# Kernel optimization log

Hardware: AMD Instinct MI355X
Metric: run time of the kernel (lower is better)

Reference implementation:

```python
import jax, jax.numpy as jnp
import numpy as np

N_NODES = 100000
N_EDGES = 1600000
N_GRAPHS = 512
F_IN = 128
HID = 128
N_CLS = 10


def setup_inputs() -> dict:
    key = jax.random.key(0)
    ks = jax.random.split(key, 12)
    x = jax.random.normal(ks[0], (N_NODES, F_IN), dtype=jnp.float32)
    edge_index = jax.random.randint(ks[1], (2, N_EDGES), 0, N_NODES, dtype=jnp.int64)
    batch = jnp.sort(jax.random.randint(ks[2], (N_NODES,), 0, N_GRAPHS, dtype=jnp.int64))
    def glorot(k, shape):
        lim = float(np.sqrt(6.0 / (shape[0] + shape[1])))
        return jax.random.uniform(k, shape, jnp.float32, -lim, lim)
    return {
        "x": x, "edge_index": edge_index, "batch": batch,
        "W1": glorot(ks[3], (F_IN, HID)), "b1": jnp.zeros((HID,), jnp.float32),
        "W2": glorot(ks[4], (HID, HID)), "b2": jnp.zeros((HID,), jnp.float32),
        "W3": glorot(ks[5], (HID, HID)), "b3": jnp.zeros((HID,), jnp.float32),
        "Wc1": glorot(ks[6], (2 * HID, HID)), "bc1": jnp.zeros((HID,), jnp.float32),
        "Wc2": glorot(ks[7], (HID, N_CLS)), "bc2": jnp.zeros((N_CLS,), jnp.float32),
    }


def _gcn_layer(h, W, b, src, dst, dinv_sqrt, norm):
    # GCNConv: transform, then symmetric-normalized aggregation with self-loops.
    h = h @ W                                    # [N, HID]
    msgs = h[src] * norm[:, None]                # gather + scale  [E, HID]
    agg = jax.ops.segment_sum(msgs, dst, num_segments=N_NODES)
    agg = agg + h * (dinv_sqrt * dinv_sqrt)[:, None]   # self-loop term (1/deg)
    return jax.nn.relu(agg + b)


def reference(x, edge_index, batch, W1, b1, W2, b2, W3, b3, Wc1, bc1, Wc2, bc2):
    src, dst = edge_index[0], edge_index[1]
    # degree including self loop (counted at aggregation target = dst)
    deg = jax.ops.segment_sum(jnp.ones((N_EDGES,), jnp.float32), dst,
                              num_segments=N_NODES) + 1.0
    dinv_sqrt = jax.lax.rsqrt(deg)
    norm = dinv_sqrt[src] * dinv_sqrt[dst]       # [E]

    h = _gcn_layer(x, W1, b1, src, dst, dinv_sqrt, norm)
    h = _gcn_layer(h, W2, b2, src, dst, dinv_sqrt, norm)
    h = _gcn_layer(h, W3, b3, src, dst, dinv_sqrt, norm)

    # mean_max pooling over graphs
    counts = jax.ops.segment_sum(jnp.ones((N_NODES,), jnp.float32), batch,
                                 num_segments=N_GRAPHS)
    sums = jax.ops.segment_sum(h, batch, num_segments=N_GRAPHS)
    g_mean = sums / jnp.maximum(counts, 1.0)[:, None]
    g_max = jax.ops.segment_max(h, batch, num_segments=N_GRAPHS)
    g_max = jnp.where(counts[:, None] > 0, g_max, 0.0)
    g = jnp.concatenate([g_mean, g_max], axis=1)  # [G, 2*HID]

    # MLP head (dropout is identity in eval mode)
    hcls = jax.nn.relu(g @ Wc1 + bc1)
    return hcls @ Wc2 + bc2                       # [G, N_CLS]
```

## Files before the change

### kernel.cpp

```cpp
#include <hip/hip_runtime.h>
#include <hip/hip_bf16.h>
#include <hip/hip_fp16.h>

#define HIDDIM 128
#define NABLK 256
#define EPB 6250
#define BCAP 5120

typedef __attribute__((ext_vector_type(8))) _Float16 half8;
typedef __attribute__((ext_vector_type(4))) float f32x4;

__device__ __forceinline__ int scan256_incl(int v, int* sbuf, int t) {
    sbuf[t] = v;
    __syncthreads();
    for (int off = 1; off < 256; off <<= 1) {
        int x = sbuf[t];
        if (t >= off) x += sbuf[t - off];
        __syncthreads();
        sbuf[t] = x;
        __syncthreads();
    }
    return sbuf[t];
}

__global__ __launch_bounds__(1024) void k_bucketA(const int* __restrict__ ei, int E,
                                                  int2* __restrict__ sortedA,
                                                  int* __restrict__ tableA, int nbuck) {
    __shared__ int2 sEdge[EPB];
    __shared__ int hist[512];
    __shared__ int sb[512];
    int t = threadIdx.x;
    int blk = blockIdx.x;
    int base = blk * EPB;
    int cnt = min(EPB, E - base);
    if (t < 512) hist[t] = 0;
    __syncthreads();
    int es[7], ed[7], rk[7];
#pragma unroll
    for (int it = 0; it < 7; ++it) {
        int i = it * 1024 + t;
        es[it] = 0; ed[it] = -1; rk[it] = 0;
        if (i < cnt) {
            es[it] = ei[base + i];
            ed[it] = ei[E + base + i];
            rk[it] = atomicAdd(&hist[ed[it] >> 8], 1);
        }
    }
    __syncthreads();
    if (t < 512) sb[t] = hist[t];
    __syncthreads();
    for (int off = 1; off < 512; off <<= 1) {
        int x = 0;
        if (t < 512) { x = sb[t]; if (t >= off) x += sb[t - off]; }
        __syncthreads();
        if (t < 512) sb[t] = x;
        __syncthreads();
    }
#pragma unroll
    for (int it = 0; it < 7; ++it) {
        if (ed[it] >= 0) {
            int b = ed[it] >> 8;
            int slot = sb[b] - hist[b] + rk[it];
            sEdge[slot] = make_int2(es[it], ed[it]);
        }
    }
    if (t <= nbuck) tableA[t * NABLK + blk] = sb[t] - hist[t];
    __syncthreads();
    for (int j = t; j < cnt; j += 1024) sortedA[base + j] = sEdge[j];
}

__global__ void k_btot(const int* __restrict__ tableA, int* __restrict__ tot) {
    __shared__ int red[4];
    int b = blockIdx.x;
    int t = threadIdx.x;
    int v = tableA[(b + 1) * NABLK + t] - tableA[b * NABLK + t];
    for (int off = 32; off; off >>= 1) v += __shfl_down(v, off, 64);
    if ((t & 63) == 0) red[t >> 6] = v;
    __syncthreads();
    if (t == 0) tot[b] = red[0] + red[1] + red[2] + red[3];
}

__global__ void k_bbase(const int* __restrict__ tot, int* __restrict__ bbase, int nbuck) {
    __shared__ int sb[512];
    int t = threadIdx.x;
    int v = (t < nbuck) ? tot[t] : 0;
    sb[t] = v;
    __syncthreads();
    for (int off = 1; off < 512; off <<= 1) {
        int x = sb[t];
        if (t >= off) x += sb[t - off];
        __syncthreads();
        sb[t] = x;
        __syncthreads();
    }
    if (t < nbuck) bbase[t] = sb[t] - v;
}

__global__ __launch_bounds__(256) void k_bucketB(const int2* __restrict__ sortedA,
                                                 const int* __restrict__ tableA,
                                                 const int* __restrict__ bbase,
                                                 int* __restrict__ csr_src,
                                                 int* __restrict__ row_off,
                                                 float* __restrict__ dinv, int N) {
    __shared__ int2 eIn[BCAP];
    __shared__ int h[256];
    __shared__ int cur[256];
    __shared__ int scanbuf[256];
    int b = blockIdx.x;
    int t = threadIdx.x;
    int s = tableA[b * NABLK + t];
    int c = tableA[(b + 1) * NABLK + t] - s;
    int rIncl = scan256_incl(c, scanbuf, t);
    int rOff = rIncl - c;
    int nE = scanbuf[255];
    for (int k = 0; k < c; ++k) {
        int p = rOff + k;
        if (p < BCAP) eIn[p] = sortedA[t * EPB + s + k];
    }
    h[t] = 0;
    __syncthreads();
    if (nE > BCAP) nE = BCAP;
    for (int j = t; j < nE; j += 256) atomicAdd(&h[eIn[j].y & 255], 1);
    __syncthreads();
    int deg = h[t];
    int nIncl = scan256_incl(deg, scanbuf, t);
    int nOff = nIncl - deg;
    int g = b * 256 + t;
    int bb = bbase[b];
    if (g < N) {
        dinv[g] = rsqrtf((float)deg + 1.0f);
        row_off[g + 1] = bb + nIncl;
        if (g == 0) row_off[0] = 0;
    }
    cur[t] = nOff;
    __syncthreads();
    for (int j = t; j < nE; j += 256) {
        int2 e = eIn[j];
        int sl = atomicAdd(&cur[e.y & 255], 1);
        csr_src[bb + sl] = e.x;
    }
}

__global__ __launch_bounds__(256) void k_wprep(const float* __restrict__ W1,
                                               const float* __restrict__ W2,
                                               const float* __restrict__ W3,
                                               __half* __restrict__ Whf,
                                               __half* __restrict__ Wdf) {
    int layer = blockIdx.x;
    const float* W = layer == 0 ? W1 : (layer == 1 ? W2 : W3);
    __half* oh = Whf + (size_t)layer * 16384;
    __half* od = Wdf + (size_t)layer * 16384;
    int t = threadIdx.x;
#pragma unroll
    for (int i = 0; i < 8; ++i) {
        int fr = t * 8 + i;
        int kk = fr >> 9;
        int jt = (fr >> 6) & 7;
        int lane = fr & 63;
        int col = jt * 16 + (lane & 15);
        int kbase = kk * 32 + ((lane >> 4) << 3);
        __half hv[8], dv[8];
#pragma unroll
        for (int e = 0; e < 8; ++e) {
            float v = W[(kbase + e) * 128 + col];
            __half h = __float2half_rn(v);
            hv[e] = h;
            dv[e] = __float2half_rn(v - __half2float(h));
        }
        *(uint4*)(oh + (size_t)fr * 8) = *(uint4*)hv;
        *(uint4*)(od + (size_t)fr * 8) = *(uint4*)dv;
    }
}

__global__ __launch_bounds__(256) void k_gemm1(const float* __restrict__ A,
                                               const __half* __restrict__ Bh,
                                               const __half* __restrict__ Bd,
                                               const float* __restrict__ dinv,
                                               __half* __restrict__ Oh, int nrows) {
    int wave = threadIdx.x >> 6, lane = threadIdx.x & 63;
    int row0 = blockIdx.x * 64 + wave * 16;
    int arow = row0 + (lane & 15);
    if (arow >= nrows) arow = nrows - 1;
    int kg = lane >> 4;
    const float* ap = A + (size_t)arow * 128 + kg * 8;
    f32x4 acc[8];
#pragma unroll
    for (int j = 0; j < 8; ++j) acc[j] = (f32x4){0.f, 0.f, 0.f, 0.f};
#pragma unroll
    for (int kk = 0; kk < 4; ++kk) {
        float4 a0 = *(const float4*)(ap + kk * 32);
        float4 a1 = *(const float4*)(ap + kk * 32 + 4);
        float av[8] = {a0.x, a0.y, a0.z, a0.w, a1.x, a1.y, a1.z, a1.w};
        half8 ah, da;
#pragma unroll
        for (int e = 0; e < 8; ++e) {
            _Float16 h = (_Float16)av[e];
            ah[e] = h;
            da[e] = (_Float16)(av[e] - (float)h);
        }
        const half8* bhp = (const half8*)(Bh + ((size_t)(kk * 8) * 64 + lane) * 8);
        const half8* bdp = (const half8*)(Bd + ((size_t)(kk * 8) * 64 + lane) * 8);
#pragma unroll
        for (int jt = 0; jt < 8; ++jt) {
            half8 bh = bhp[jt * 64];
            half8 bd = bdp[jt * 64];
            acc[jt] = __builtin_amdgcn_mfma_f32_16x16x32_f16(ah, bh, acc[jt], 0, 0, 0);
            acc[jt] = __builtin_amdgcn_mfma_f32_16x16x32_f16(da, bh, acc[jt], 0, 0, 0);
            acc[jt] = __builtin_amdgcn_mfma_f32_16x16x32_f16(ah, bd, acc[jt], 0, 0, 0);
        }
    }
    int ocol = lane & 15;
    int orow_base = row0 + (lane >> 4) * 4;
#pragma unroll
    for (int r = 0; r < 4; ++r) {
        int orow = orow_base + r;
        if (orow < nrows) {
            float dv = dinv[orow];
#pragma unroll
            for (int jt = 0; jt < 8; ++jt)
                Oh[(size_t)orow * 128 + jt * 16 + ocol] = __float2half_rn(acc[jt][r] * dv);
        }
    }
}

__global__ __launch_bounds__(256) void k_gemm16(const __half* __restrict__ A,
                                                const __half* __restrict__ Bh,
                                                const __half* __restrict__ Bd,
                                                const float* __restrict__ dinv,
                                                __half* __restrict__ Oh, int nrows) {
    int wave = threadIdx.x >> 6, lane = threadIdx.x & 63;
    int row0 = blockIdx.x * 64 + wave * 16;
    int arow = row0 + (lane & 15);
    if (arow >= nrows) arow = nrows - 1;
    int kg = lane >> 4;
    const __half* ap = A + (size_t)arow * 128 + kg * 8;
    f32x4 acc[8];
#pragma unroll
    for (int j = 0; j < 8; ++j) acc[j] = (f32x4){0.f, 0.f, 0.f, 0.f};
#pragma unroll
    for (int kk = 0; kk < 4; ++kk) {
        half8 ah = *(const half8*)(ap + kk * 32);
        const half8* bhp = (const half8*)(Bh + ((size_t)(kk * 8) * 64 + lane) * 8);
        const half8* bdp = (const half8*)(Bd + ((size_t)(kk * 8) * 64 + lane) * 8);
#pragma unroll
        for (int jt = 0; jt < 8; ++jt) {
            half8 bh = bhp[jt * 64];
            half8 bd = bdp[jt * 64];
            acc[jt] = __builtin_amdgcn_mfma_f32_16x16x32_f16(ah, bh, acc[jt], 0, 0, 0);
            acc[jt] = __builtin_amdgcn_mfma_f32_16x16x32_f16(ah, bd, acc[jt], 0, 0, 0);
        }
    }
    int ocol = lane & 15;
    int orow_base = row0 + (lane >> 4) * 4;
#pragma unroll
    for (int r = 0; r < 4; ++r) {
        int orow = orow_base + r;
        if (orow < nrows) {
            float dv = dinv[orow];
#pragma unroll
            for (int jt = 0; jt < 8; ++jt)
                Oh[(size_t)orow * 128 + jt * 16 + ocol] = __float2half_rn(acc[jt][r] * dv);
        }
    }
}

__global__ __launch_bounds__(256) void k_agg(const __half* __restrict__ hHs,
                                             const int* __restrict__ row_off,
                                             const int* __restrict__ csr_src,
                                             const float* __restrict__ dinv,
                                             const float* __restrict__ bias,
                                             __half* __restrict__ outH, int n) {
    int node = blockIdx.x * 4 + (threadIdx.x >> 6);
    int lane = threadIdx.x & 63;
    if (node >= n) return;
    int half = lane >> 5;
    int q = lane & 31;
    float dd = dinv[node];
    int s = row_off[node], e = row_off[node + 1];
    int cnt = e - s;
    const int* __restrict__ cp = csr_src + s;
    float4 acc = make_float4(0.f, 0.f, 0.f, 0.f);
    for (int t = 0; t < cnt; t += 8) {
        int idx[4];
#pragma unroll
        for (int p = 0; p < 4; ++p) {
            int tt = t + 2 * p + half;
            bool ok = tt < cnt;
            int raw = cp[ok ? tt : 0];
            idx[p] = ok ? raw : n;
        }
        uint2 w[4];
#pragma unroll
        for (int p = 0; p < 4; ++p)
            w[p] = *(const uint2*)((const char*)hHs + (((size_t)(unsigned)idx[p]) << 8) + ((unsigned)q << 3));
#pragma unroll
        for (int p = 0; p < 4; ++p) {
            float2 f0 = __half22float2(*(const __half2*)&w[p].x);
            float2 f1 = __half22float2(*(const __half2*)&w[p].y);
            acc.x += f0.x;
            acc.y += f0.y;
            acc.z += f1.x;
            acc.w += f1.y;
        }
    }
    acc.x += __shfl_xor(acc.x, 32);
    acc.y += __shfl_xor(acc.y, 32);
    acc.z += __shfl_xor(acc.z, 32);
    acc.w += __shfl_xor(acc.w, 32);
    if (half == 0) {
        uint2 sw = *(const uint2*)((const char*)hHs + ((size_t)(unsigned)node << 8) + ((unsigned)q << 3));
        float2 s0 = __half22float2(*(const __half2*)&sw.x);
        float2 s1 = __half22float2(*(const __half2*)&sw.y);
        float4 bb = *(const float4*)(bias + q * 4);
        __half o[4];
        o[0] = __float2half_rn(fmaxf(fmaf(dd, acc.x + s0.x, bb.x), 0.f));
        o[1] = __float2half_rn(fmaxf(fmaf(dd, acc.y + s0.y, bb.y), 0.f));
        o[2] = __float2half_rn(fmaxf(fmaf(dd, acc.z + s1.x, bb.z), 0.f));
        o[3] = __float2half_rn(fmaxf(fmaf(dd, acc.w + s1.y, bb.w), 0.f));
        *(uint2*)(outH + (size_t)node * 128 + q * 4) = *(uint2*)o;
    }
}

__global__ void k_pool(const __half* __restrict__ h, const int* __restrict__ batch,
                       float* __restrict__ gsum, float* __restrict__ gmax,
                       int* __restrict__ gcnt, int n) {
    int t = threadIdx.x;
    int start = blockIdx.x * 64;
    if (start >= n) return;
    int end = min(start + 64, n);
    int cur = batch[start];
    float s = 0.f, m = 0.f;
    int c = 0;
    for (int i = start; i < end; ++i) {
        int g = batch[i];
        if (g != cur) {
            atomicAdd(&gsum[cur * 128 + t], s);
            atomicMax((int*)&gmax[cur * 128 + t], __float_as_int(m));
            if (t == 0) atomicAdd(&gcnt[cur], c);
            s = 0.f; m = 0.f; c = 0; cur = g;
        }
        float v = __half2float(h[(size_t)i * 128 + t]);
        s += v;
        m = fmaxf(m, v);
        c++;
    }
    atomicAdd(&gsum[cur * 128 + t], s);
    atomicMax((int*)&gmax[cur * 128 + t], __float_as_int(m));
    if (t == 0) atomicAdd(&gcnt[cur], c);
}

__global__ void k_head(const float* __restrict__ gsum, const float* __restrict__ gmax,
                       const int* __restrict__ gcnt, const float* __restrict__ Wc1,
                       const float* __restrict__ bc1, const float* __restrict__ Wc2,
                       const float* __restrict__ bc2, float* __restrict__ out, int G) {
    __shared__ float gv[256];
    __shared__ float hc[128];
    int g = blockIdx.x;
    if (g >= G) return;
    int t = threadIdx.x;
    float c = (float)gcnt[g];
    float inv = 1.0f / fmaxf(c, 1.0f);
    gv[t] = gsum[g * 128 + t] * inv;
    gv[128 + t] = gmax[g * 128 + t];
    __syncthreads();
    float a = bc1[t];
#pragma unroll 8
    for (int k = 0; k < 256; ++k) a = fmaf(gv[k], Wc1[k * 128 + t], a);
    hc[t] = fmaxf(a, 0.f);
    __syncthreads();
    if (t < 10) {
        float o = bc2[t];
        for (int k = 0; k < 128; ++k) o = fmaf(hc[k], Wc2[k * 10 + t], o);
        out[g * 10 + t] = o;
    }
}

extern "C" void kernel_launch(void* const* d_in, const int* in_sizes, int n_in,
                              void* d_out, int out_size, void* d_ws, size_t ws_size,
                              hipStream_t stream) {
    const float* x   = (const float*)d_in[0];
    const int*   ei  = (const int*)d_in[1];
    const int*   bat = (const int*)d_in[2];
    const float* W1  = (const float*)d_in[3];
    const float* b1  = (const float*)d_in[4];
    const float* W2  = (const float*)d_in[5];
    const float* b2  = (const float*)d_in[6];
    const float* W3  = (const float*)d_in[7];
    const float* b3  = (const float*)d_in[8];
    const float* Wc1 = (const float*)d_in[9];
    const float* bc1 = (const float*)d_in[10];
    const float* Wc2 = (const float*)d_in[11];
    const float* bc2 = (const float*)d_in[12];
    float* out = (float*)d_out;

    const int N = in_sizes[0] / HIDDIM;
    const int E = in_sizes[1] / 2;
    const int G = out_size / 10;
    const int nbuck = (N + 255) >> 8;

    char* ws = (char*)d_ws;
    size_t off = 0;
    auto take = [&](size_t bytes) -> char* {
        char* p = ws + off;
        off += (bytes + 255) & ~(size_t)255;
        return p;
    };
    __half* aggH    = (__half*)take((size_t)N * HIDDIM * 2);
    int2*  sortedA  = (int2*)aggH;
    __half* hHs     = (__half*)take(((size_t)N + 1) * HIDDIM * 2);
    float* dinv     = (float*)take((size_t)N * 4);
    int*   row_off  = (int*)take(((size_t)N + 1) * 4);
    int*   tableA   = (int*)take((size_t)(nbuck + 1) * NABLK * 4);
    int*   tot      = (int*)take(512 * 4);
    int*   bbase    = (int*)take(512 * 4);
    int*   csr_src  = (int*)take((size_t)E * 4);
    float* gsum     = (float*)take((size_t)G * HIDDIM * 4);
    float* gmax     = (float*)take((size_t)G * HIDDIM * 4);
    int*   gcnt     = (int*)take((size_t)G * 4);
    __half* Whf     = (__half*)take((size_t)3 * 16384 * 2);
    __half* Wdf     = (__half*)take((size_t)3 * 16384 * 2);

    hipMemsetAsync(gsum, 0, (size_t)G * HIDDIM * 4, stream);
    hipMemsetAsync(gmax, 0, (size_t)G * HIDDIM * 4, stream);
    hipMemsetAsync(gcnt, 0, (size_t)G * 4, stream);
    hipMemsetAsync(hHs + (size_t)N * HIDDIM, 0, HIDDIM * 2, stream);

    k_bucketA<<<NABLK, 1024, 0, stream>>>(ei, E, sortedA, tableA, nbuck);
    k_btot<<<nbuck, 256, 0, stream>>>(tableA, tot);
    k_bbase<<<1, 512, 0, stream>>>(tot, bbase, nbuck);
    k_bucketB<<<nbuck, 256, 0, stream>>>(sortedA, tableA, bbase, csr_src, row_off, dinv, N);
    k_wprep<<<3, 256, 0, stream>>>(W1, W2, W3, Whf, Wdf);

    int gb = (N + 63) / 64;
    int ab = (N + 3) / 4;
    k_gemm1<<<gb, 256, 0, stream>>>(x, Whf, Wdf, dinv, hHs, N);
    k_agg<<<ab, 256, 0, stream>>>(hHs, row_off, csr_src, dinv, b1, aggH, N);
    k_gemm16<<<gb, 256, 0, stream>>>(aggH, Whf + 16384, Wdf + 16384, dinv, hHs, N);
    k_agg<<<ab, 256, 0, stream>>>(hHs, row_off, csr_src, dinv, b2, aggH, N);
    k_gemm16<<<gb, 256, 0, stream>>>(aggH, Whf + 32768, Wdf + 32768, dinv, hHs, N);
    k_agg<<<ab, 256, 0, stream>>>(hHs, row_off, csr_src, dinv, b3, aggH, N);

    k_pool<<<(N + 63) / 64, 128, 0, stream>>>(aggH, bat, gsum, gmax, gcnt, N);
    k_head<<<G, 128, 0, stream>>>(gsum, gmax, gcnt, Wc1, bc1, Wc2, bc2, out, G);
}
```

Measured before the change: 353.3 us.

## Pad CSR rows to multiples of eight with fixed per-bucket stride

Each node's CSR neighbor list is padded to a multiple of 8 using the zero sentinel row N, and each 256-node bucket gets a fixed-stride region of csr_src. This removes the global bucket-total and prefix-scan kernels (k_btot, k_bbase). The aggregation loop also loses its per-element bounds checks and reads an (offset, padded count) pair per node. In exchange it reads extra padded zero rows and relies on each bucket fitting in BSTRIDE entries.

```diff
diff --git a/kernel.cpp b/kernel.cpp
--- a/kernel.cpp
+++ b/kernel.cpp
@@ -6,6 +6,7 @@
 #define NABLK 256
 #define EPB 6250
 #define BCAP 5120
+#define BSTRIDE 7168
 
 typedef __attribute__((ext_vector_type(8))) _Float16 half8;
 typedef __attribute__((ext_vector_type(4))) float f32x4;
@@ -69,38 +70,10 @@
     for (int j = t; j < cnt; j += 1024) sortedA[base + j] = sEdge[j];
 }
 
-__global__ void k_btot(const int* __restrict__ tableA, int* __restrict__ tot) {
-    __shared__ int red[4];
-    int b = blockIdx.x;
-    int t = threadIdx.x;
-    int v = tableA[(b + 1) * NABLK + t] - tableA[b * NABLK + t];
-    for (int off = 32; off; off >>= 1) v += __shfl_down(v, off, 64);
-    if ((t & 63) == 0) red[t >> 6] = v;
-    __syncthreads();
-    if (t == 0) tot[b] = red[0] + red[1] + red[2] + red[3];
-}
-
-__global__ void k_bbase(const int* __restrict__ tot, int* __restrict__ bbase, int nbuck) {
-    __shared__ int sb[512];
-    int t = threadIdx.x;
-    int v = (t < nbuck) ? tot[t] : 0;
-    sb[t] = v;
-    __syncthreads();
-    for (int off = 1; off < 512; off <<= 1) {
-        int x = sb[t];
-        if (t >= off) x += sb[t - off];
-        __syncthreads();
-        sb[t] = x;
-        __syncthreads();
-    }
-    if (t < nbuck) bbase[t] = sb[t] - v;
-}
-
 __global__ __launch_bounds__(256) void k_bucketB(const int2* __restrict__ sortedA,
                                                  const int* __restrict__ tableA,
-                                                 const int* __restrict__ bbase,
                                                  int* __restrict__ csr_src,
-                                                 int* __restrict__ row_off,
+                                                 int2* __restrict__ row2,
                                                  float* __restrict__ dinv, int N) {
     __shared__ int2 eIn[BCAP];
     __shared__ int h[256];
@@ -123,22 +96,23 @@
     for (int j = t; j < nE; j += 256) atomicAdd(&h[eIn[j].y & 255], 1);
     __syncthreads();
     int deg = h[t];
-    int nIncl = scan256_incl(deg, scanbuf, t);
-    int nOff = nIncl - deg;
+    int pdeg = (deg + 7) & ~7;
+    int pIncl = scan256_incl(pdeg, scanbuf, t);
+    int pOff = pIncl - pdeg;
     int g = b * 256 + t;
-    int bb = bbase[b];
+    int gbase = b * BSTRIDE;
     if (g < N) {
         dinv[g] = rsqrtf((float)deg + 1.0f);
-        row_off[g + 1] = bb + nIncl;
-        if (g == 0) row_off[0] = 0;
-    }
-    cur[t] = nOff;
+        row2[g] = make_int2(gbase + pOff, pdeg);
+    }
+    cur[t] = pOff;
     __syncthreads();
     for (int j = t; j < nE; j += 256) {
         int2 e = eIn[j];
         int sl = atomicAdd(&cur[e.y & 255], 1);
-        csr_src[bb + sl] = e.x;
-    }
+        csr_src[gbase + sl] = e.x;
+    }
+    for (int j = deg; j < pdeg; ++j) csr_src[gbase + pOff + j] = N;
 }
 
 __global__ __launch_bounds__(256) void k_wprep(const float* __restrict__ W1,
@@ -265,7 +239,7 @@
 }
 
 __global__ __launch_bounds__(256) void k_agg(const __half* __restrict__ hHs,
-                                             const int* __restrict__ row_off,
+                                             const int2* __restrict__ row2,
                                              const int* __restrict__ csr_src,
                                              const float* __restrict__ dinv,
                                              const float* __restrict__ bias,
@@ -275,28 +249,27 @@
     if (node >= n) return;
     int half = lane >> 5;
     int q = lane & 31;
+    unsigned qo = (unsigned)q << 3;
     float dd = dinv[node];
-    int s = row_off[node], e = row_off[node + 1];
-    int cnt = e - s;
-    const int* __restrict__ cp = csr_src + s;
+    int2 ro = row2[node];
+    const int* __restrict__ cp = csr_src + ro.x;
+    int iters = ro.y >> 3;
     float4 acc = make_float4(0.f, 0.f, 0.f, 0.f);
-    for (int t = 0; t < cnt; t += 8) {
-        int idx[4];
+    for (int it = 0; it < iters; ++it) {
+        int i0 = cp[half];
+        int i1 = cp[2 + half];
+        int i2 = cp[4 + half];
+        int i3 = cp[6 + half];
+        cp += 8;
+        uint2 w0 = *(const uint2*)((const char*)hHs + (((size_t)(unsigned)i0) << 8) + qo);
+        uint2 w1 = *(const uint2*)((const char*)hHs + (((size_t)(unsigned)i1) << 8) + qo);
+        uint2 w2 = *(const uint2*)((const char*)hHs + (((size_t)(unsigned)i2) << 8) + qo);
+        uint2 w3 = *(const uint2*)((const char*)hHs + (((size_t)(unsigned)i3) << 8) + qo);
 #pragma unroll
         for (int p = 0; p < 4; ++p) {
-            int tt = t + 2 * p + half;
-            bool ok = tt < cnt;
-            int raw = cp[ok ? tt : 0];
-            idx[p] = ok ? raw : n;
-        }
-        uint2 w[4];
-#pragma unroll
-        for (int p = 0; p < 4; ++p)
-            w[p] = *(const uint2*)((const char*)hHs + (((size_t)(unsigned)idx[p]) << 8) + ((unsigned)q << 3));
-#pragma unroll
-        for (int p = 0; p < 4; ++p) {
-            float2 f0 = __half22float2(*(const __half2*)&w[p].x);
-            float2 f1 = __half22float2(*(const __half2*)&w[p].y);
+            uint2 w = p == 0 ? w0 : (p == 1 ? w1 : (p == 2 ? w2 : w3));
+            float2 f0 = __half22float2(*(const __half2*)&w.x);
+            float2 f1 = __half22float2(*(const __half2*)&w.y);
             acc.x += f0.x;
             acc.y += f0.y;
             acc.z += f1.x;
@@ -308,7 +281,7 @@
     acc.z += __shfl_xor(acc.z, 32);
     acc.w += __shfl_xor(acc.w, 32);
     if (half == 0) {
-        uint2 sw = *(const uint2*)((const char*)hHs + ((size_t)(unsigned)node << 8) + ((unsigned)q << 3));
+        uint2 sw = *(const uint2*)((const char*)hHs + ((size_t)(unsigned)node << 8) + qo);
         float2 s0 = __half22float2(*(const __half2*)&sw.x);
         float2 s1 = __half22float2(*(const __half2*)&sw.y);
         float4 bb = *(const float4*)(bias + q * 4);
@@ -409,11 +382,9 @@
     int2*  sortedA  = (int2*)aggH;
     __half* hHs     = (__half*)take(((size_t)N + 1) * HIDDIM * 2);
     float* dinv     = (float*)take((size_t)N * 4);
-    int*   row_off  = (int*)take(((size_t)N + 1) * 4);
+    int2*  row2     = (int2*)take((size_t)N * 8);
     int*   tableA   = (int*)take((size_t)(nbuck + 1) * NABLK * 4);
-    int*   tot      = (int*)take(512 * 4);
-    int*   bbase    = (int*)take(512 * 4);
-    int*   csr_src  = (int*)take((size_t)E * 4);
+    int*   csr_src  = (int*)take((size_t)nbuck * BSTRIDE * 4);
     float* gsum     = (float*)take((size_t)G * HIDDIM * 4);
     float* gmax     = (float*)take((size_t)G * HIDDIM * 4);
     int*   gcnt     = (int*)take((size_t)G * 4);
@@ -426,19 +397,17 @@
     hipMemsetAsync(hHs + (size_t)N * HIDDIM, 0, HIDDIM * 2, stream);
 
     k_bucketA<<<NABLK, 1024, 0, stream>>>(ei, E, sortedA, tableA, nbuck);
-    k_btot<<<nbuck, 256, 0, stream>>>(tableA, tot);
-    k_bbase<<<1, 512, 0, stream>>>(tot, bbase, nbuck);
-    k_bucketB<<<nbuck, 256, 0, stream>>>(sortedA, tableA, bbase, csr_src, row_off, dinv, N);
+    k_bucketB<<<nbuck, 256, 0, stream>>>(sortedA, tableA, csr_src, row2, dinv, N);
     k_wprep<<<3, 256, 0, stream>>>(W1, W2, W3, Whf, Wdf);
 
     int gb = (N + 63) / 64;
     int ab = (N + 3) / 4;
     k_gemm1<<<gb, 256, 0, stream>>>(x, Whf, Wdf, dinv, hHs, N);
-    k_agg<<<ab, 256, 0, stream>>>(hHs, row_off, csr_src, dinv, b1, aggH, N);
+    k_agg<<<ab, 256, 0, stream>>>(hHs, row2, csr_src, dinv, b1, aggH, N);
     k_gemm16<<<gb, 256, 0, stream>>>(aggH, Whf + 16384, Wdf + 16384, dinv, hHs, N);
-    k_agg<<<ab, 256, 0, stream>>>(hHs, row_off, csr_src, dinv, b2, aggH, N);
+    k_agg<<<ab, 256, 0, stream>>>(hHs, row2, csr_src, dinv, b2, aggH, N);
     k_gemm16<<<gb, 256, 0, stream>>>(aggH, Whf + 32768, Wdf + 32768, dinv, hHs, N);
-    k_agg<<<ab, 256, 0, stream>>>(hHs, row_off, csr_src, dinv, b3, aggH, N);
+    k_agg<<<ab, 256, 0, stream>>>(hHs, row2, csr_src, dinv, b3, aggH, N);
 
     k_pool<<<(N + 63) / 64, 128, 0, stream>>>(aggH, bat, gsum, gmax, gcnt, N);
     k_head<<<G, 128, 0, stream>>>(gsum, gmax, gcnt, Wc1, bc1, Wc2, bc2, out, G);
```

Result: no change. 354.4 us (+0.3%).
